# Kernel tuning notes

Measured on AMD Instinct MI355X. Metric: run time of the kernel, lower is better.

Reference implementation:

```python
import jax, jax.numpy as jnp
import numpy as np

HIDDEN = 2048
N_HEADS = 16
HEAD_DIM = HIDDEN // N_HEADS
BATCH = 2
SEQ = 2048
N_CP = max(8, int(HIDDEN * HIDDEN / 128.9))  # 32540 control points


def _spline_to_weight(cp, out_dim, in_dim):
    # Reconstruct full weight matrix by sampling the control-point curve at
    # out_dim*in_dim evenly spaced parameter values (piecewise-linear spline eval).
    n = cp.shape[0]
    t = jnp.linspace(0.0, 1.0, out_dim * in_dim)
    xp = jnp.linspace(0.0, 1.0, n)
    return jnp.interp(t, xp, cp).reshape(out_dim, in_dim)


def setup_inputs() -> dict:
    key = jax.random.key(0)
    ks = jax.random.split(key, 5)
    hidden_states = jax.random.normal(ks[0], (BATCH, SEQ, HIDDEN), dtype=jnp.float32)
    cp_q = jax.random.normal(ks[1], (N_CP,), dtype=jnp.float32) * 0.02
    cp_k = jax.random.normal(ks[2], (N_CP,), dtype=jnp.float32) * 0.02
    cp_v = jax.random.normal(ks[3], (N_CP,), dtype=jnp.float32) * 0.02
    cp_o = jax.random.normal(ks[4], (N_CP,), dtype=jnp.float32) * 0.02
    # additive causal mask [1,1,S,S]
    causal = jnp.tril(jnp.ones((SEQ, SEQ), dtype=bool))
    attention_mask = jnp.where(causal, 0.0, -1e9).astype(jnp.float32)[None, None]
    return {
        'hidden_states': hidden_states,
        'cp_q': cp_q, 'cp_k': cp_k, 'cp_v': cp_v, 'cp_o': cp_o,
        'attention_mask': attention_mask,
    }


def reference(hidden_states, cp_q, cp_k, cp_v, cp_o, attention_mask):
    B, S, H = hidden_states.shape
    q_w = _spline_to_weight(cp_q, H, H)
    k_w = _spline_to_weight(cp_k, H, H)
    v_w = _spline_to_weight(cp_v, H, H)
    o_w = _spline_to_weight(cp_o, H, H)

    # F.linear(x, W) == x @ W.T
    q = (hidden_states @ q_w.T).reshape(B, S, N_HEADS, HEAD_DIM).transpose(0, 2, 1, 3)
    k = (hidden_states @ k_w.T).reshape(B, S, N_HEADS, HEAD_DIM).transpose(0, 2, 1, 3)
    v = (hidden_states @ v_w.T).reshape(B, S, N_HEADS, HEAD_DIM).transpose(0, 2, 1, 3)

    scale = 1.0 / np.sqrt(HEAD_DIM).astype(np.float32)
    scores = jnp.einsum('bhqd,bhkd->bhqk', q, k) * scale + attention_mask
    probs = jax.nn.softmax(scores.astype(jnp.float32), axis=-1).astype(q.dtype)
    attn = jnp.einsum('bhqk,bhkd->bhqd', probs, v)
    attn = attn.transpose(0, 2, 1, 3).reshape(B, S, H)
    return attn @ o_w.T
```

## Files before the change

kernel.cpp:

```cpp
#include <hip/hip_runtime.h>
#include <stdint.h>

typedef unsigned short u16;
typedef __bf16 bf16x8 __attribute__((ext_vector_type(8)));
typedef float f32x4 __attribute__((ext_vector_type(4)));
typedef u16 u16x4 __attribute__((ext_vector_type(4)));

#define MFMA16(a, b, c) __builtin_amdgcn_mfma_f32_16x16x32_bf16((a), (b), (c), 0, 0, 0)

__device__ __forceinline__ u16 f2bf(float f) {
  uint32_t u = __builtin_bit_cast(uint32_t, f);
  u += 0x7FFFu + ((u >> 16) & 1u);
  return (u16)(u >> 16);
}
__device__ __forceinline__ bf16x8 cvt8(f32x4 lo, f32x4 hi) {
  union { u16 u[8]; bf16x8 v; } r;
#pragma unroll
  for (int j = 0; j < 4; j++) { r.u[j] = f2bf(lo[j]); r.u[4 + j] = f2bf(hi[j]); }
  return r.v;
}
__device__ __forceinline__ void gld_lds16(const void* g, void* l) {
  __builtin_amdgcn_global_load_lds(
      (const __attribute__((address_space(1))) uint32_t*)g,
      (__attribute__((address_space(3))) uint32_t*)l, 16, 0, 0);
}

__global__ void prep_kernel(const float* __restrict__ x, const float* __restrict__ cpq,
                            const float* __restrict__ cpk, const float* __restrict__ cpv,
                            const float* __restrict__ cpo, u16* __restrict__ xb,
                            u16* __restrict__ Wqkv, u16* __restrict__ Wo,
                            int n, double factor) {
  int blk = blockIdx.x;
  if (blk < 65536) {
    int idx = blk * 256 + threadIdx.x;
    int w = idx >> 22;
    int i = idx & 4194303;
    const float* cp = (w == 0) ? cpq : (w == 1) ? cpk : (w == 2) ? cpv : cpo;
    double u = (double)i * factor;
    int i0 = (int)u;
    if (i0 > n - 2) i0 = n - 2;
    float fr = (float)(u - (double)i0);
    float f0 = cp[i0], f1 = cp[i0 + 1];
    u16 bv = f2bf(f0 + fr * (f1 - f0));
    if (w < 3) Wqkv[idx] = bv; else Wo[i] = bv;
  } else {
    size_t i = ((size_t)(blk - 65536) * 256 + threadIdx.x) * 8;
    const f32x4* p = (const f32x4*)(x + i);
    *(bf16x8*)(xb + i) = cvt8(p[0], p[1]);
  }
}

template <int MODE>
__global__ __launch_bounds__(256, 2)
void gemm_bt(const u16* __restrict__ A, const u16* __restrict__ B,
             u16* __restrict__ oQ, u16* __restrict__ oK, u16* __restrict__ oV,
             float* __restrict__ oC) {
  constexpr int KD = 2048;
  __shared__ __align__(16) u16 As[128 * 64];
  __shared__ __align__(16) u16 Bs[128 * 64];
  const int tid = threadIdx.x;
  const int wave = tid >> 6, lane = tid & 63, quad = lane >> 4, l16 = lane & 15;
  const int wm = wave & 1, wn = wave >> 1;
  const int m0 = blockIdx.y * 128, n0 = blockIdx.x * 128;

  size_t aoff[4], boff[4];
  int lslot[4];
#pragma unroll
  for (int b = 0; b < 4; b++) {
    int s = wave * 256 + b * 64 + lane;
    int r = s >> 3, c = s & 7, gc = c ^ (r & 7);
    lslot[b] = s * 16;
    aoff[b] = (size_t)(m0 + r) * (KD * 2) + gc * 16;
    boff[b] = (size_t)(n0 + r) * (KD * 2) + gc * 16;
  }
  const char* Ab = (const char*)A;
  const char* Bb = (const char*)B;
  char* AsB = (char*)As;
  char* BsB = (char*)Bs;

  f32x4 acc[4][4];
  const f32x4 fz = {0.f, 0.f, 0.f, 0.f};
#pragma unroll
  for (int i = 0; i < 4; i++)
#pragma unroll
    for (int j = 0; j < 4; j++) acc[i][j] = fz;

  for (int kt = 0; kt < KD / 64; ++kt) {
    if (kt) __syncthreads();
#pragma unroll
    for (int b = 0; b < 4; b++) {
      gld_lds16(Ab + aoff[b], AsB + lslot[b]);
      gld_lds16(Bb + boff[b], BsB + lslot[b]);
      aoff[b] += 128;
      boff[b] += 128;
    }
    __syncthreads();
#pragma unroll
    for (int t = 0; t < 2; t++) {
      bf16x8 af[4], bfb[4];
#pragma unroll
      for (int i = 0; i < 4; i++) {
        int row = wm * 64 + i * 16 + l16;
        int ch = (t * 4 + quad) ^ (row & 7);
        af[i] = *(const bf16x8*)(AsB + row * 128 + ch * 16);
      }
#pragma unroll
      for (int j = 0; j < 4; j++) {
        int row = wn * 64 + j * 16 + l16;
        int ch = (t * 4 + quad) ^ (row & 7);
        bfb[j] = *(const bf16x8*)(BsB + row * 128 + ch * 16);
      }
#pragma unroll
      for (int i = 0; i < 4; i++)
#pragma unroll
        for (int j = 0; j < 4; j++) acc[i][j] = MFMA16(af[i], bfb[j], acc[i][j]);
    }
  }

  if (MODE == 0) {
    const float qscale = 0.08838834764831845f;
#pragma unroll
    for (int j = 0; j < 4; j++) {
      int nb = n0 + wn * 64 + j * 16;
      int sel = nb >> 11;
      int h = (nb >> 7) & 15;
      int d = (nb & 127) + l16;
#pragma unroll
      for (int i = 0; i < 4; i++) {
        int mrow = m0 + wm * 64 + i * 16 + quad * 4;
        int bq = mrow >> 11, srow = mrow & 2047;
        if (sel == 2) {
          u16x4 pk = {f2bf(acc[i][j][0]), f2bf(acc[i][j][1]),
                      f2bf(acc[i][j][2]), f2bf(acc[i][j][3])};
          *(u16x4*)&oV[(size_t)(((bq << 4) + h) * 128 + d) * 2048 + srow] = pk;
        } else if (sel == 0) {
          int base = ((bq << 4) + h) * 2048;
#pragma unroll
          for (int r = 0; r < 4; r++)
            oQ[(size_t)(base + srow + r) * 128 + d] = f2bf(acc[i][j][r] * qscale);
        } else {
          int base = ((bq << 4) + h) * 2048;
#pragma unroll
          for (int r = 0; r < 4; r++)
            oK[(size_t)(base + srow + r) * 128 + d] = f2bf(acc[i][j][r]);
        }
      }
    }
  } else {
#pragma unroll
    for (int j = 0; j < 4; j++) {
      int col = n0 + wn * 64 + j * 16 + l16;
#pragma unroll
      for (int i = 0; i < 4; i++) {
        int mrow = m0 + wm * 64 + i * 16 + quad * 4;
#pragma unroll
        for (int r = 0; r < 4; r++) oC[(size_t)(mrow + r) * 2048 + col] = acc[i][j][r];
      }
    }
  }
}

__global__ __launch_bounds__(256, 2)
void flash_attn(const u16* __restrict__ Q, const u16* __restrict__ Kg,
                const u16* __restrict__ Vt, u16* __restrict__ attn) {
  __shared__ __align__(16) u16 Ks[64 * 128];
  __shared__ __align__(16) u16 Vs[128 * 64];
  __shared__ __align__(16) u16 Ps[128 * 72];
  const int tid = threadIdx.x;
  const int wave = tid >> 6, lane = tid & 63, quad = lane >> 4, l16 = lane & 15;
  const int L = blockIdx.x;
  const int bh = L & 31;
  const int qi = (L >> 5) & 7;
  const int qt = (L >= 256) ? (15 - qi) : qi;
  const int q0 = qt * 128;
  const u16* Qb = Q + (size_t)bh * 2048 * 128;
  const u16* Kb = Kg + (size_t)bh * 2048 * 128;
  const u16* Vb = Vt + (size_t)bh * 128 * 2048;

  bf16x8 qf[2][4];
#pragma unroll
  for (int i = 0; i < 2; i++) {
    int row = q0 + wave * 32 + i * 16 + l16;
#pragma unroll
    for (int t = 0; t < 4; t++)
      qf[i][t] = *(const bf16x8*)(Qb + (size_t)row * 128 + t * 32 + quad * 8);
  }

  f32x4 o_acc[2][8];
  const f32x4 fz = {0.f, 0.f, 0.f, 0.f};
#pragma unroll
  for (int i = 0; i < 2; i++)
#pragma unroll
    for (int j = 0; j < 8; j++) o_acc[i][j] = fz;
  float l_i[2] = {0.f, 0.f};

  int koff[4], voff[4], lslot[4];
#pragma unroll
  for (int b = 0; b < 4; b++) {
    int s = wave * 256 + b * 64 + lane;
    lslot[b] = s * 16;
    {
      int r = s >> 4, c = s & 15;
      int gc = (c & 8) | ((c & 7) ^ (r & 7));
      koff[b] = r * 256 + gc * 16;
    }
    {
      int r = s >> 3, c = s & 7;
      int gc = c ^ (r & 7);
      voff[b] = r * 4096 + gc * 16;
    }
  }
  const char* KbB = (const char*)Kb;
  const char* VbB = (const char*)Vb;
  char* KsB = (char*)Ks;
  char* VsB = (char*)Vs;

  const int ktmax = 2 * qt + 1;

  for (int kt = 0; kt <= ktmax; ++kt) {
    const int k0 = kt * 64;
    if (kt) __syncthreads();
#pragma unroll
    for (int b = 0; b < 4; b++) {
      gld_lds16(KbB + (size_t)k0 * 256 + koff[b], KsB + lslot[b]);
      gld_lds16(VbB + (size_t)k0 * 2 + voff[b], VsB + lslot[b]);
    }
    __syncthreads();

    f32x4 st[2][4];
#pragma unroll
    for (int i = 0; i < 2; i++)
#pragma unroll
      for (int j = 0; j < 4; j++) st[i][j] = fz;
#pragma unroll
    for (int j = 0; j < 4; j++) {
      int rowk = j * 16 + l16;
#pragma unroll
      for (int t = 0; t < 4; t++) {
        int cc = t * 4 + quad;
        int ch = (cc & 8) | ((cc & 7) ^ (rowk & 7));
        bf16x8 kfr = *(const bf16x8*)(KsB + rowk * 256 + ch * 16);
        st[0][j] = MFMA16(kfr, qf[0][t], st[0][j]);
        st[1][j] = MFMA16(kfr, qf[1][t], st[1][j]);
      }
    }

    const bool do_mask = (kt >= 2 * qt);
#pragma unroll
    for (int i = 0; i < 2; i++) {
      const int qg = q0 + wave * 32 + i * 16 + l16;
      float lacc = 0.f;
#pragma unroll
      for (int j = 0; j < 4; j++) {
        float p[4];
#pragma unroll
        for (int r = 0; r < 4; r++) {
          float v = st[i][j][r];
          if (do_mask && (k0 + j * 16 + quad * 4 + r > qg)) v = -1e30f;
          p[r] = __expf(v);
        }
        lacc += (p[0] + p[1]) + (p[2] + p[3]);
        u16x4 pk = {f2bf(p[0]), f2bf(p[1]), f2bf(p[2]), f2bf(p[3])};
        *(u16x4*)&Ps[(wave * 32 + i * 16 + l16) * 72 + j * 16 + quad * 4] = pk;
      }
      l_i[i] += lacc;
    }

#pragma unroll
    for (int t = 0; t < 2; t++) {
      bf16x8 af0 = *(const bf16x8*)((char*)Ps + (wave * 32 + l16) * 144 + (t * 32 + quad * 8) * 2);
      bf16x8 af1 = *(const bf16x8*)((char*)Ps + (wave * 32 + 16 + l16) * 144 + (t * 32 + quad * 8) * 2);
#pragma unroll
      for (int j = 0; j < 8; j++) {
        int vrow = j * 16 + l16;
        int ch = (t * 4 + quad) ^ (vrow & 7);
        bf16x8 bfr = *(const bf16x8*)(VsB + vrow * 128 + ch * 16);
        o_acc[0][j] = MFMA16(af0, bfr, o_acc[0][j]);
        o_acc[1][j] = MFMA16(af1, bfr, o_acc[1][j]);
      }
    }
  }

  const int bb = bh >> 4, h = bh & 15;
#pragma unroll
  for (int i = 0; i < 2; i++) {
    float rs = l_i[i];
    rs += __shfl_xor(rs, 16);
    rs += __shfl_xor(rs, 32);
    float inv = 1.f / rs;
#pragma unroll
    for (int r = 0; r < 4; r++) {
      float invr = __shfl(inv, (lane & 48) | (quad * 4 + r), 64);
      int srow = q0 + wave * 32 + i * 16 + quad * 4 + r;
      size_t base = ((size_t)(bb * 2048 + srow)) * 2048 + h * 128;
#pragma unroll
      for (int j = 0; j < 8; j++) attn[base + j * 16 + l16] = f2bf(o_acc[i][j][r] * invr);
    }
  }
}

extern "C" void kernel_launch(void* const* d_in, const int* in_sizes, int n_in,
                              void* d_out, int out_size, void* d_ws, size_t ws_size,
                              hipStream_t stream) {
  (void)n_in; (void)out_size; (void)ws_size;
  const float* x = (const float*)d_in[0];
  const float* cpq = (const float*)d_in[1];
  const float* cpk = (const float*)d_in[2];
  const float* cpv = (const float*)d_in[3];
  const float* cpo = (const float*)d_in[4];
  float* out = (float*)d_out;
  const int ncp = in_sizes[1];
  const double factor = (double)(ncp - 1) / 4194303.0;

  char* ws = (char*)d_ws;
  u16* Wqkv = (u16*)(ws);
  u16* At   = (u16*)(ws);
  u16* Wo = (u16*)(ws + 25165824);
  u16* Qp = (u16*)(ws + 33554432);
  u16* Kp = (u16*)(ws + 50331648);
  u16* Vp = (u16*)(ws + 67108864);
  u16* xb = (u16*)d_out;

  prep_kernel<<<dim3(69632), dim3(256), 0, stream>>>(x, cpq, cpk, cpv, cpo, xb, Wqkv, Wo, ncp, factor);
  gemm_bt<0><<<dim3(48, 32), dim3(256), 0, stream>>>(xb, Wqkv, Qp, Kp, Vp, nullptr);
  flash_attn<<<dim3(512), dim3(256), 0, stream>>>(Qp, Kp, Vp, At);
  gemm_bt<1><<<dim3(16, 32), dim3(256), 0, stream>>>(At, Wo, nullptr, nullptr, nullptr, out);
}
```

Before: 345.4 us.

## Replace QKV projection GEMM with 256x128-tile triple-buffered 512-thread kernel

Adds a dedicated QKV projection kernel that uses 512-thread blocks, 256x128 output tiles, K-step 32 and a three-stage LDS ring filled by direct global-to-LDS loads with swizzled addressing. It also remaps the block index so tiles sharing a weight column panel run together, aiming for better L2 reuse. The goal is to hide global load latency and raise MFMA utilisation compared with the earlier 128x128 double-buffered GEMM. The trade-offs are higher register pressure from launch bounds of 4 blocks per CU, and the need for the epilogue's Q scaling and V-transposed stores to still match what the flash-attention kernel expects.

```diff
diff --git a/kernel.cpp b/kernel.cpp
--- a/kernel.cpp
+++ b/kernel.cpp
@@ -50,6 +50,137 @@
   }
 }
 
+__global__ __launch_bounds__(512, 4)
+void gemm_qkv(const u16* __restrict__ A, const u16* __restrict__ B,
+              u16* __restrict__ oQ, u16* __restrict__ oK, u16* __restrict__ oV) {
+  constexpr int KD = 2048;
+  constexpr int NT = KD / 32;
+  __shared__ __align__(16) u16 As[3 * 256 * 32];
+  __shared__ __align__(16) u16 Bs[3 * 128 * 32];
+  const int tid = threadIdx.x;
+  const int wave = tid >> 6, lane = tid & 63, quad = lane >> 4, l16 = lane & 15;
+  const int wm = wave >> 1, wn = wave & 1;
+  const int z = blockIdx.x;
+  const int mt = (z >> 4) & 15;
+  const int nt = ((z >> 8) << 4) | (z & 15);
+  const int m0 = mt * 256, n0 = nt * 128;
+
+  const int sA0 = wave * 128 + lane;
+  const int sA1 = sA0 + 64;
+  const int sB = wave * 64 + lane;
+  auto mkoff = [&](int s, int rbase) -> size_t {
+    int r = s >> 2, c = s & 3;
+    int gc = c ^ ((r ^ (r >> 2)) & 3);
+    return (size_t)(rbase + r) * (KD * 2) + gc * 16;
+  };
+  const size_t aoff0 = mkoff(sA0, m0);
+  const size_t aoff1 = mkoff(sA1, m0);
+  const size_t boff = mkoff(sB, n0);
+  const int lA0 = sA0 * 16, lA1 = sA1 * 16, lB = sB * 16;
+
+  int roffA[4], roffB[4];
+#pragma unroll
+  for (int mi = 0; mi < 4; mi++) {
+    int row = wm * 64 + mi * 16 + l16;
+    roffA[mi] = row * 64 + ((quad ^ ((row ^ (row >> 2)) & 3)) * 16);
+  }
+#pragma unroll
+  for (int nj = 0; nj < 4; nj++) {
+    int row = wn * 64 + nj * 16 + l16;
+    roffB[nj] = row * 64 + ((quad ^ ((row ^ (row >> 2)) & 3)) * 16);
+  }
+
+  const char* Ab = (const char*)A;
+  const char* Bb = (const char*)B;
+  char* AsB = (char*)As;
+  char* BsB = (char*)Bs;
+
+  f32x4 acc[4][4];
+  const f32x4 fz = {0.f, 0.f, 0.f, 0.f};
+#pragma unroll
+  for (int i = 0; i < 4; i++)
+#pragma unroll
+    for (int j = 0; j < 4; j++) acc[i][j] = fz;
+
+  auto STAGE = [&](int ba, int bb, size_t kb) {
+    gld_lds16(Ab + aoff0 + kb, AsB + ba + lA0);
+    gld_lds16(Ab + aoff1 + kb, AsB + ba + lA1);
+    gld_lds16(Bb + boff + kb, BsB + bb + lB);
+  };
+
+#define QKV_BODY(T, CUR, NX2)                                                 \
+  do {                                                                        \
+    if ((T) + 2 < NT)                                                         \
+      STAGE((NX2) * 16384, (NX2) * 8192, (size_t)((T) + 2) * 64);             \
+    bf16x8 af[4], bfv[4];                                                     \
+    _Pragma("unroll") for (int mi = 0; mi < 4; mi++)                          \
+        af[mi] = *(const bf16x8*)(AsB + (CUR) * 16384 + roffA[mi]);           \
+    _Pragma("unroll") for (int nj = 0; nj < 4; nj++)                          \
+        bfv[nj] = *(const bf16x8*)(BsB + (CUR) * 8192 + roffB[nj]);           \
+    __builtin_amdgcn_s_setprio(1);                                            \
+    _Pragma("unroll") for (int mi = 0; mi < 4; mi++)                          \
+        _Pragma("unroll") for (int nj = 0; nj < 4; nj++)                      \
+            acc[mi][nj] = MFMA16(af[mi], bfv[nj], acc[mi][nj]);               \
+    __builtin_amdgcn_s_setprio(0);                                            \
+    if ((T) + 2 < NT)                                                         \
+      asm volatile("s_waitcnt vmcnt(3)" ::: "memory");                        \
+    else if ((T) + 1 < NT)                                                    \
+      asm volatile("s_waitcnt vmcnt(0)" ::: "memory");                        \
+    if ((T) + 1 < NT) {                                                       \
+      __builtin_amdgcn_s_barrier();                                           \
+      __builtin_amdgcn_sched_barrier(0);                                      \
+    }                                                                         \
+  } while (0)
+
+  STAGE(0, 0, 0);
+  STAGE(16384, 8192, 64);
+  asm volatile("s_waitcnt vmcnt(3)" ::: "memory");
+  __builtin_amdgcn_s_barrier();
+  __builtin_amdgcn_sched_barrier(0);
+
+  for (int t = 0; t < 63; t += 3) {
+    QKV_BODY(t, 0, 2);
+    QKV_BODY(t + 1, 1, 0);
+    QKV_BODY(t + 2, 2, 1);
+  }
+  QKV_BODY(63, 0, 2);
+#undef QKV_BODY
+
+  const int sel = n0 >> 11;
+  const int h = (n0 >> 7) & 15;
+  const int bq = m0 >> 11;
+  const int sb2 = m0 & 2047;
+  if (sel == 2) {
+#pragma unroll
+    for (int nj = 0; nj < 4; nj++) {
+      int d = wn * 64 + nj * 16 + l16;
+      size_t colb = ((size_t)((bq << 4) + h) * 128 + d) * 2048;
+#pragma unroll
+      for (int mi = 0; mi < 4; mi++) {
+        int srow = sb2 + wm * 64 + mi * 16 + quad * 4;
+        u16x4 pk = {f2bf(acc[mi][nj][0]), f2bf(acc[mi][nj][1]),
+                    f2bf(acc[mi][nj][2]), f2bf(acc[mi][nj][3])};
+        *(u16x4*)&oV[colb + srow] = pk;
+      }
+    }
+  } else {
+    u16* __restrict__ o = (sel == 0) ? oQ : oK;
+    const float sc = (sel == 0) ? 0.08838834764831845f : 1.0f;
+    const int base = ((bq << 4) + h) * 2048;
+#pragma unroll
+    for (int nj = 0; nj < 4; nj++) {
+      int d = wn * 64 + nj * 16 + l16;
+#pragma unroll
+      for (int mi = 0; mi < 4; mi++) {
+        int srow = sb2 + wm * 64 + mi * 16 + quad * 4;
+#pragma unroll
+        for (int r = 0; r < 4; r++)
+          o[(size_t)(base + srow + r) * 128 + d] = f2bf(acc[mi][nj][r] * sc);
+      }
+    }
+  }
+}
+
 template <int MODE>
 __global__ __launch_bounds__(256, 2)
 void gemm_bt(const u16* __restrict__ A, const u16* __restrict__ B,
@@ -322,7 +453,7 @@
   u16* xb = (u16*)d_out;
 
   prep_kernel<<<dim3(69632), dim3(256), 0, stream>>>(x, cpq, cpk, cpv, cpo, xb, Wqkv, Wo, ncp, factor);
-  gemm_bt<0><<<dim3(48, 32), dim3(256), 0, stream>>>(xb, Wqkv, Qp, Kp, Vp, nullptr);
+  gemm_qkv<<<dim3(768), dim3(512), 0, stream>>>(xb, Wqkv, Qp, Kp, Vp);
   flash_attn<<<dim3(512), dim3(256), 0, stream>>>(Qp, Kp, Vp, At);
   gemm_bt<1><<<dim3(16, 32), dim3(256), 0, stream>>>(At, Wo, nullptr, nullptr, nullptr, out);
 }
```

Measured after the change: 361.0 us. 1.05x slower.

## Add dedicated QKV GEMM with 128x256 tiles, triple-buffered LDS and XCD swizzle

Applied to the files above, without the earlier changes.

Replaces the generic QKV projection GEMM with a new 512-thread kernel that computes 128x256 output tiles. It uses a three-stage global-to-LDS pipeline with explicit vmcnt waits, raised wave priority around the MFMA blocks, and a block-index remap that groups tiles per XCD. The aim is to hide load latency and get more operand reuse per block. In exchange it uses much more LDS (144KB per block), which limits occupancy, and adds hand-tuned wait counts that must match the number of loads in flight.

```diff
diff --git a/kernel.cpp b/kernel.cpp
--- a/kernel.cpp
+++ b/kernel.cpp
@@ -50,6 +50,139 @@
   }
 }
 
+__global__ __launch_bounds__(512, 2)
+void gemm_qkv(const u16* __restrict__ A, const u16* __restrict__ B,
+              u16* __restrict__ oQ, u16* __restrict__ oK, u16* __restrict__ oV) {
+  __shared__ __align__(16) u16 As[3 * 128 * 64];
+  __shared__ __align__(16) u16 Bs[3 * 256 * 64];
+  const int tid = threadIdx.x;
+  const int wave = tid >> 6, lane = tid & 63, quad = lane >> 4, l16 = lane & 15;
+  const int wm = wave & 1, wn = wave >> 1;
+
+  const int z = blockIdx.x;
+  const int wg = (z & 7) * 96 + (z >> 3);
+  const int mt = wg / 24, nt = wg - mt * 24;
+  const int m0 = mt * 128, n0 = nt * 256;
+
+  size_t aoffg[2], boffg[4];
+  int lA[2], lB[4];
+#pragma unroll
+  for (int u = 0; u < 2; u++) {
+    int s = u * 512 + tid, r = s >> 3, c = s & 7, gc = c ^ (r & 7);
+    lA[u] = s * 16;
+    aoffg[u] = (size_t)(m0 + r) * 4096 + gc * 16;
+  }
+#pragma unroll
+  for (int u = 0; u < 4; u++) {
+    int s = u * 512 + tid, r = s >> 3, c = s & 7, gc = c ^ (r & 7);
+    lB[u] = s * 16;
+    boffg[u] = (size_t)(n0 + r) * 4096 + gc * 16;
+  }
+
+  int roA[4], roB[4];
+#pragma unroll
+  for (int mi = 0; mi < 4; mi++) {
+    int row = wm * 64 + mi * 16 + l16;
+    roA[mi] = row * 128 + ((quad ^ (row & 7)) * 16);
+  }
+#pragma unroll
+  for (int nj = 0; nj < 4; nj++) {
+    int row = wn * 64 + nj * 16 + l16;
+    roB[nj] = row * 128 + ((quad ^ (row & 7)) * 16);
+  }
+
+  const char* Ab = (const char*)A;
+  const char* Bb = (const char*)B;
+  char* AsB = (char*)As;
+  char* BsB = (char*)Bs;
+
+  f32x4 acc[4][4];
+  const f32x4 fz = {0.f, 0.f, 0.f, 0.f};
+#pragma unroll
+  for (int i = 0; i < 4; i++)
+#pragma unroll
+    for (int j = 0; j < 4; j++) acc[i][j] = fz;
+
+#define QKV_STAGE(TT, NX)                                                     \
+  do {                                                                        \
+    size_t kb = (size_t)(TT) * 128;                                           \
+    gld_lds16(Ab + aoffg[0] + kb, AsB + (NX) * 16384 + lA[0]);                \
+    gld_lds16(Ab + aoffg[1] + kb, AsB + (NX) * 16384 + lA[1]);                \
+    gld_lds16(Bb + boffg[0] + kb, BsB + (NX) * 32768 + lB[0]);                \
+    gld_lds16(Bb + boffg[1] + kb, BsB + (NX) * 32768 + lB[1]);                \
+    gld_lds16(Bb + boffg[2] + kb, BsB + (NX) * 32768 + lB[2]);                \
+    gld_lds16(Bb + boffg[3] + kb, BsB + (NX) * 32768 + lB[3]);                \
+  } while (0)
+
+#define QKV_BODY(T, CUR, NX, STG, WM)                                         \
+  do {                                                                        \
+    if (STG) QKV_STAGE((T) + 2, NX);                                          \
+    _Pragma("unroll") for (int t = 0; t < 2; t++) {                           \
+      bf16x8 af[4], bfv[4];                                                   \
+      _Pragma("unroll") for (int mi = 0; mi < 4; mi++)                        \
+          af[mi] = *(const bf16x8*)(AsB + (CUR) * 16384 + (roA[mi] ^ (t * 64))); \
+      _Pragma("unroll") for (int nj = 0; nj < 4; nj++)                        \
+          bfv[nj] = *(const bf16x8*)(BsB + (CUR) * 32768 + (roB[nj] ^ (t * 64))); \
+      __builtin_amdgcn_s_setprio(1);                                          \
+      _Pragma("unroll") for (int mi = 0; mi < 4; mi++)                        \
+          _Pragma("unroll") for (int nj = 0; nj < 4; nj++)                    \
+              acc[mi][nj] = MFMA16(af[mi], bfv[nj], acc[mi][nj]);             \
+      __builtin_amdgcn_s_setprio(0);                                          \
+    }                                                                         \
+    if ((WM) == 6) asm volatile("s_waitcnt vmcnt(6)" ::: "memory");           \
+    else if ((WM) == 0) asm volatile("s_waitcnt vmcnt(0)" ::: "memory");      \
+    if ((WM) >= 0) {                                                          \
+      __builtin_amdgcn_s_barrier();                                           \
+      __builtin_amdgcn_sched_barrier(0);                                      \
+    }                                                                         \
+  } while (0)
+
+  QKV_STAGE(0, 0);
+  QKV_STAGE(1, 1);
+  asm volatile("s_waitcnt vmcnt(6)" ::: "memory");
+  __builtin_amdgcn_s_barrier();
+  __builtin_amdgcn_sched_barrier(0);
+
+  for (int t = 0; t < 30; t += 3) {
+    QKV_BODY(t, 0, 2, true, 6);
+    QKV_BODY(t + 1, 1, 0, true, 6);
+    QKV_BODY(t + 2, 2, 1, true, 6);
+  }
+  QKV_BODY(30, 0, 2, false, 0);
+  QKV_BODY(31, 1, 0, false, -1);
+#undef QKV_BODY
+#undef QKV_STAGE
+
+  const float qscale = 0.08838834764831845f;
+#pragma unroll
+  for (int j = 0; j < 4; j++) {
+    int nb = n0 + wn * 64 + j * 16;
+    int sel = nb >> 11;
+    int h = (nb >> 7) & 15;
+    int d = (nb & 127) + l16;
+#pragma unroll
+    for (int i = 0; i < 4; i++) {
+      int mrow = m0 + wm * 64 + i * 16 + quad * 4;
+      int bq = mrow >> 11, srow = mrow & 2047;
+      if (sel == 2) {
+        u16x4 pk = {f2bf(acc[i][j][0]), f2bf(acc[i][j][1]),
+                    f2bf(acc[i][j][2]), f2bf(acc[i][j][3])};
+        *(u16x4*)&oV[(size_t)(((bq << 4) + h) * 128 + d) * 2048 + srow] = pk;
+      } else if (sel == 0) {
+        int base = ((bq << 4) + h) * 2048;
+#pragma unroll
+        for (int r = 0; r < 4; r++)
+          oQ[(size_t)(base + srow + r) * 128 + d] = f2bf(acc[i][j][r] * qscale);
+      } else {
+        int base = ((bq << 4) + h) * 2048;
+#pragma unroll
+        for (int r = 0; r < 4; r++)
+          oK[(size_t)(base + srow + r) * 128 + d] = f2bf(acc[i][j][r]);
+      }
+    }
+  }
+}
+
 template <int MODE>
 __global__ __launch_bounds__(256, 2)
 void gemm_bt(const u16* __restrict__ A, const u16* __restrict__ B,
@@ -322,7 +455,7 @@
   u16* xb = (u16*)d_out;
 
   prep_kernel<<<dim3(69632), dim3(256), 0, stream>>>(x, cpq, cpk, cpv, cpo, xb, Wqkv, Wo, ncp, factor);
-  gemm_bt<0><<<dim3(48, 32), dim3(256), 0, stream>>>(xb, Wqkv, Qp, Kp, Vp, nullptr);
+  gemm_qkv<<<dim3(768), dim3(512), 0, stream>>>(xb, Wqkv, Qp, Kp, Vp);
   flash_attn<<<dim3(512), dim3(256), 0, stream>>>(Qp, Kp, Vp, At);
   gemm_bt<1><<<dim3(16, 32), dim3(256), 0, stream>>>(At, Wo, nullptr, nullptr, nullptr, out);
 }
```

Measured after the change: 356.1 us. 3.1% more time.

## Double-buffer K/V tiles in flash attention, prefetching the next tile during compute

Applied to the files above, without the earlier changes.

K and V shared-memory tiles are now double-buffered. The next tile's global-to-LDS loads are issued before computing on the current tile, with a single barrier at the end of each iteration, so load latency overlaps with MFMA work instead of stalling at a barrier each step. The P staging row stride also changes from 72 to 68 elements, and s_setprio is raised around the MFMA pairs. LDS use grows by about 32KB per block, which may cut occupancy at 2 blocks per CU. The padding change may also alter bank-conflict behaviour and the alignment of the 16-byte reads (136-byte rows are not 16-byte aligned). The loop reads the prefetched buffer after a barrier with no explicit wait on the asynchronous loads, so it relies on the barrier handling vmcnt.

```diff
diff --git a/kernel.cpp b/kernel.cpp
--- a/kernel.cpp
+++ b/kernel.cpp
@@ -163,9 +163,9 @@
 __global__ __launch_bounds__(256, 2)
 void flash_attn(const u16* __restrict__ Q, const u16* __restrict__ Kg,
                 const u16* __restrict__ Vt, u16* __restrict__ attn) {
-  __shared__ __align__(16) u16 Ks[64 * 128];
-  __shared__ __align__(16) u16 Vs[128 * 64];
-  __shared__ __align__(16) u16 Ps[128 * 72];
+  __shared__ __align__(16) u16 Ks[2][64 * 128];
+  __shared__ __align__(16) u16 Vs[2][128 * 64];
+  __shared__ __align__(16) u16 Ps[128 * 68];
   const int tid = threadIdx.x;
   const int wave = tid >> 6, lane = tid & 63, quad = lane >> 4, l16 = lane & 15;
   const int L = blockIdx.x;
@@ -217,15 +217,26 @@
 
   const int ktmax = 2 * qt + 1;
 
+#pragma unroll
+  for (int b = 0; b < 4; b++) {
+    gld_lds16(KbB + koff[b], KsB + lslot[b]);
+    gld_lds16(VbB + voff[b], VsB + lslot[b]);
+  }
+  __syncthreads();
+
   for (int kt = 0; kt <= ktmax; ++kt) {
-    const int k0 = kt * 64;
-    if (kt) __syncthreads();
-#pragma unroll
-    for (int b = 0; b < 4; b++) {
-      gld_lds16(KbB + (size_t)k0 * 256 + koff[b], KsB + lslot[b]);
-      gld_lds16(VbB + (size_t)k0 * 2 + voff[b], VsB + lslot[b]);
-    }
-    __syncthreads();
+    const int cur = kt & 1;
+    if (kt < ktmax) {
+      const size_t k1 = (size_t)(kt + 1) * 64;
+      const int nx = (cur ^ 1) * 16384;
+#pragma unroll
+      for (int b = 0; b < 4; b++) {
+        gld_lds16(KbB + k1 * 256 + koff[b], KsB + nx + lslot[b]);
+        gld_lds16(VbB + k1 * 2 + voff[b], VsB + nx + lslot[b]);
+      }
+    }
+    const char* Kcur = KsB + cur * 16384;
+    const char* Vcur = VsB + cur * 16384;
 
     f32x4 st[2][4];
 #pragma unroll
@@ -239,12 +250,15 @@
       for (int t = 0; t < 4; t++) {
         int cc = t * 4 + quad;
         int ch = (cc & 8) | ((cc & 7) ^ (rowk & 7));
-        bf16x8 kfr = *(const bf16x8*)(KsB + rowk * 256 + ch * 16);
+        bf16x8 kfr = *(const bf16x8*)(Kcur + rowk * 256 + ch * 16);
+        __builtin_amdgcn_s_setprio(1);
         st[0][j] = MFMA16(kfr, qf[0][t], st[0][j]);
         st[1][j] = MFMA16(kfr, qf[1][t], st[1][j]);
-      }
-    }
-
+        __builtin_amdgcn_s_setprio(0);
+      }
+    }
+
+    const int k0 = kt * 64;
     const bool do_mask = (kt >= 2 * qt);
 #pragma unroll
     for (int i = 0; i < 2; i++) {
@@ -261,24 +275,28 @@
         }
         lacc += (p[0] + p[1]) + (p[2] + p[3]);
         u16x4 pk = {f2bf(p[0]), f2bf(p[1]), f2bf(p[2]), f2bf(p[3])};
-        *(u16x4*)&Ps[(wave * 32 + i * 16 + l16) * 72 + j * 16 + quad * 4] = pk;
+        *(u16x4*)&Ps[(wave * 32 + i * 16 + l16) * 68 + j * 16 + quad * 4] = pk;
       }
       l_i[i] += lacc;
     }
 
 #pragma unroll
     for (int t = 0; t < 2; t++) {
-      bf16x8 af0 = *(const bf16x8*)((char*)Ps + (wave * 32 + l16) * 144 + (t * 32 + quad * 8) * 2);
-      bf16x8 af1 = *(const bf16x8*)((char*)Ps + (wave * 32 + 16 + l16) * 144 + (t * 32 + quad * 8) * 2);
+      bf16x8 af0 = *(const bf16x8*)((char*)Ps + (wave * 32 + l16) * 136 + (t * 32 + quad * 8) * 2);
+      bf16x8 af1 = *(const bf16x8*)((char*)Ps + (wave * 32 + 16 + l16) * 136 + (t * 32 + quad * 8) * 2);
 #pragma unroll
       for (int j = 0; j < 8; j++) {
         int vrow = j * 16 + l16;
         int ch = (t * 4 + quad) ^ (vrow & 7);
-        bf16x8 bfr = *(const bf16x8*)(VsB + vrow * 128 + ch * 16);
+        bf16x8 bfr = *(const bf16x8*)(Vcur + vrow * 128 + ch * 16);
+        __builtin_amdgcn_s_setprio(1);
         o_acc[0][j] = MFMA16(af0, bfr, o_acc[0][j]);
         o_acc[1][j] = MFMA16(af1, bfr, o_acc[1][j]);
-      }
-    }
+        __builtin_amdgcn_s_setprio(0);
+      }
+    }
+
+    __syncthreads();
   }
 
   const int bb = bh >> 4, h = bh & 15;
```

Result: slower. 365.1 us (+5.7%).
